# Kernel tuning notes

Hardware: AMD Instinct MI355X
Metric: run time of the kernel (lower is better)

Reference implementation:

```python
import jax, jax.numpy as jnp
import numpy as np

B, N, D, S, ITERS = 64, 2048, 256, 8, 3
SCALE = D ** -0.5
EPS_LN = 1e-5

def _ln(x, g, b):
    m = jnp.mean(x, axis=-1, keepdims=True)
    v = jnp.var(x, axis=-1, keepdims=True)
    return (x - m) / jnp.sqrt(v + EPS_LN) * g + b

def setup_inputs() -> dict:
    key = jax.random.key(0)
    ks = jax.random.split(key, 20)
    s = D ** -0.5
    f32 = jnp.float32
    return dict(
        x=jax.random.normal(ks[0], (B, N, D), f32),
        noise=jax.random.normal(ks[1], (B, S, D), f32),
        slots_mu=jax.random.normal(ks[2], (1, 1, D), f32),
        slots_sigma=jax.random.normal(ks[3], (1, 1, D), f32),
        Wq=jax.random.normal(ks[4], (D, D), f32) * s, bq=jnp.zeros((D,), f32),
        Wk=jax.random.normal(ks[5], (D, D), f32) * s, bk=jnp.zeros((D,), f32),
        Wv=jax.random.normal(ks[6], (D, D), f32) * s, bv=jnp.zeros((D,), f32),
        W_ih=jax.random.normal(ks[7], (3 * D, D), f32) * s, b_ih=jnp.zeros((3 * D,), f32),
        W_hh=jax.random.normal(ks[8], (3 * D, D), f32) * s, b_hh=jnp.zeros((3 * D,), f32),
        W1=jax.random.normal(ks[9], (D, D), f32) * s, b1=jnp.zeros((D,), f32),
        W2=jax.random.normal(ks[10], (D, D), f32) * s, b2=jnp.zeros((D,), f32),
        g_in=jnp.ones((D,), f32), be_in=jnp.zeros((D,), f32),
        g_sl=jnp.ones((D,), f32), be_sl=jnp.zeros((D,), f32),
        g_ff=jnp.ones((D,), f32), be_ff=jnp.zeros((D,), f32),
    )

def reference(x, noise, slots_mu, slots_sigma, Wq, bq, Wk, bk, Wv, bv,
              W_ih, b_ih, W_hh, b_hh, W1, b1, W2, b2,
              g_in, be_in, g_sl, be_sl, g_ff, be_ff):
    # slot init: mu + softplus(sigma) * noise  -> [B,S,D]
    slots = slots_mu + jax.nn.softplus(slots_sigma) * noise
    xn = _ln(x, g_in, be_in)
    k = xn @ Wk.T + bk  # [B,N,D]
    v = xn @ Wv.T + bv
    for _ in range(ITERS):
        prev = slots
        q = _ln(slots, g_sl, be_sl) @ Wq.T + bq  # [B,S,D]
        logits = jnp.einsum('bsd,bnd->bsn', q, k) * SCALE
        attn = jax.nn.softmax(logits, axis=-1) + 1e-8  # softmax over inputs, as in source
        attn = attn / jnp.sum(attn, axis=-1, keepdims=True)
        updates = jnp.einsum('bsn,bnd->bsd', attn, v)
        # GRUCell(input=updates, hidden=prev); torch gate order r,z,n
        gi = updates @ W_ih.T + b_ih
        gh = prev @ W_hh.T + b_hh
        ir, iz, i_n = jnp.split(gi, 3, axis=-1)
        hr, hz, h_n = jnp.split(gh, 3, axis=-1)
        r = jax.nn.sigmoid(ir + hr)
        z = jax.nn.sigmoid(iz + hz)
        n = jnp.tanh(i_n + r * h_n)
        slots = (1.0 - z) * n + z * prev
        # residual MLP
        h = jax.nn.relu(_ln(slots, g_ff, be_ff) @ W1.T + b1)
        slots = slots + (h @ W2.T + b2)
    return slots
```

## Files before the change

### kernel.cpp

```cpp
#include <hip/hip_runtime.h>
#include <cstddef>


#define BB 64
#define NN 2048
#define DD 256
#define NCH 8
#define CHK 256
#define NITER 3
#define XPITCH 264

typedef unsigned short u16;
typedef unsigned int u32;
typedef _Float16 h2 __attribute__((ext_vector_type(2)));
typedef _Float16 h4 __attribute__((ext_vector_type(4)));

#if defined(__has_builtin)
#if __has_builtin(__builtin_amdgcn_fdot2)
#define HAS_FDOT2 1
#endif
#endif

#ifdef HAS_FDOT2
#define FDOT2(a,b,c) __builtin_amdgcn_fdot2((a),(b),(c),false)
#else
#define FDOT2(a,b,c) fmaf((float)(a).y,(float)(b).y, fmaf((float)(a).x,(float)(b).x,(c)))
#endif

__device__ __forceinline__ h2 u2h2(u32 v){ union{u32 u; h2 h;} c; c.u=v; return c.h; }

__global__ __launch_bounds__(256) void kA(const float* __restrict__ x, const float* __restrict__ g_in,
                                          const float* __restrict__ be_in, u16* __restrict__ xn,
                                          const float* __restrict__ noise, const float* __restrict__ mu,
                                          const float* __restrict__ sig, float* __restrict__ S,
                                          const float* __restrict__ Wq, const float* __restrict__ Wk,
                                          const float* __restrict__ bq, const float* __restrict__ Wih,
                                          const float* __restrict__ Wv, const float* __restrict__ bv,
                                          const float* __restrict__ bih,
                                          float* __restrict__ Wqk, float* __restrict__ bqk,
                                          float* __restrict__ Wihv, float* __restrict__ bihv){
  __shared__ float col[256];
  const int t = threadIdx.x;
  const int blk = blockIdx.x;
  if(blk < 256){
    col[t] = Wq[t*256 + blk];
    __syncthreads();
    float acc = 0.f;
    #pragma unroll 4
    for(int j=0;j<256;j++) acc += col[j]*Wk[j*256+t];
    Wqk[blk*256+t] = acc * 0.0625f;
  } else if(blk < 1024){
    int c = blk - 256;
    col[t] = Wih[c*256+t];
    __syncthreads();
    float acc = 0.f;
    #pragma unroll 4
    for(int j=0;j<256;j++) acc += col[j]*Wv[j*256+t];
    Wihv[(size_t)c*256+t] = acc;
  } else if(blk < 1536){
    int i = (blk-1024)*256 + t;
    float sg = sig[t];
    float sp = fmaxf(sg, 0.f) + log1pf(expf(-fabsf(sg)));
    S[i] = mu[t] + sp * noise[i];
  } else if(blk == 1536){
    float acc = 0.f;
    for(int j=0;j<256;j++) acc += bq[j]*Wk[j*256+t];
    bqk[t] = acc * 0.0625f;
  } else if(blk == 1537){
    for(int c=t;c<768;c+=256){
      float acc = 0.f;
      for(int j=0;j<256;j++) acc += Wih[c*256+j]*bv[j];
      bihv[c] = acc + bih[c];
    }
  } else {
    int wave = t>>6, lane = t&63;
    size_t row = (size_t)(blk-1538)*4 + wave;
    float4 v = *(const float4*)(x + row*256 + lane*4);
    float s1 = v.x+v.y+v.z+v.w;
    float s2 = v.x*v.x + v.y*v.y + v.z*v.z + v.w*v.w;
    #pragma unroll
    for(int off=1; off<64; off<<=1){ s1 += __shfl_xor(s1,off); s2 += __shfl_xor(s2,off); }
    float m = s1*(1.f/256.f);
    float var = s2*(1.f/256.f) - m*m;
    float rs = rsqrtf(var + 1e-5f);
    float4 gg = *(const float4*)(g_in + lane*4);
    float4 bb = *(const float4*)(be_in + lane*4);
    union { h4 h; ushort4 s4; } pk;
    pk.h[0] = (_Float16)((v.x-m)*rs*gg.x + bb.x);
    pk.h[1] = (_Float16)((v.y-m)*rs*gg.y + bb.y);
    pk.h[2] = (_Float16)((v.z-m)*rs*gg.z + bb.z);
    pk.h[3] = (_Float16)((v.w-m)*rs*gg.w + bb.w);
    *(ushort4*)(xn + row*256 + lane*4) = pk.s4;
  }
}

__global__ __launch_bounds__(256) void kB(const float* __restrict__ Wihv, const float* __restrict__ Whh,
                                          const float* __restrict__ W1, const float* __restrict__ W2,
                                          float* __restrict__ WihvT, float* __restrict__ WhhT,
                                          float* __restrict__ W1T, float* __restrict__ W2T,
                                          const float* __restrict__ S0, const float* __restrict__ g_sl,
                                          const float* __restrict__ be_sl, const float* __restrict__ Wqk,
                                          const float* __restrict__ bqk, float* __restrict__ Qq){
  __shared__ float tile[64][65];
  __shared__ float lnA[8][256];
  const int blk = blockIdx.x, t = threadIdx.x;
  if(blk < 128){
    const float* src; float* dst; int R, C, tb;
    if(blk < 48){ src=Wihv; dst=WihvT; R=768; C=256; tb=blk; }
    else if(blk < 96){ src=Whh; dst=WhhT; R=768; C=256; tb=blk-48; }
    else if(blk < 112){ src=W1; dst=W1T; R=256; C=256; tb=blk-96; }
    else { src=W2; dst=W2T; R=256; C=256; tb=blk-112; }
    const int tilesC = C/64;
    const int r0 = (tb/tilesC)*64, c0 = (tb%tilesC)*64;
    const int x = t&63, y = t>>6;
    #pragma unroll
    for(int k=0;k<16;k++) tile[y*16+k][x] = src[(size_t)(r0+y*16+k)*C + c0+x];
    __syncthreads();
    #pragma unroll
    for(int k=0;k<16;k++) dst[(size_t)(c0+y*16+k)*R + r0+x] = tile[x][y*16+k];
    return;
  }
  const int w = t>>6, l = t&63;
  const int r0 = (blk-128)*8;
  #pragma unroll
  for(int rr=0; rr<2; rr++){
    int r = w*2 + rr;
    float4 v = *(const float4*)(S0 + (size_t)(r0+r)*256 + l*4);
    float s1 = v.x+v.y+v.z+v.w;
    float s2 = v.x*v.x+v.y*v.y+v.z*v.z+v.w*v.w;
    #pragma unroll
    for(int off=1; off<64; off<<=1){ s1 += __shfl_xor(s1,off); s2 += __shfl_xor(s2,off); }
    float m = s1*(1.f/256.f);
    float var = s2*(1.f/256.f) - m*m;
    float rs = rsqrtf(var + 1e-5f);
    float4 gg = *(const float4*)(g_sl + l*4);
    float4 bb = *(const float4*)(be_sl + l*4);
    float4 o;
    o.x=(v.x-m)*rs*gg.x+bb.x; o.y=(v.y-m)*rs*gg.y+bb.y;
    o.z=(v.z-m)*rs*gg.z+bb.z; o.w=(v.w-m)*rs*gg.w+bb.w;
    *(float4*)(&lnA[r][l*4]) = o;
  }
  __syncthreads();
  const int c4 = l*4;
  float acc[2][4] = {};
  #pragma unroll 2
  for(int k=0;k<256;k++){
    float4 wv = *(const float4*)(Wqk + (size_t)k*256 + c4);
    float a0 = lnA[2*w][k], a1 = lnA[2*w+1][k];
    acc[0][0]+=a0*wv.x; acc[0][1]+=a0*wv.y; acc[0][2]+=a0*wv.z; acc[0][3]+=a0*wv.w;
    acc[1][0]+=a1*wv.x; acc[1][1]+=a1*wv.y; acc[1][2]+=a1*wv.z; acc[1][3]+=a1*wv.w;
  }
  float4 bq4 = *(const float4*)(bqk + c4);
  #pragma unroll
  for(int rr=0; rr<2; rr++){
    float4 o;
    o.x=acc[rr][0]+bq4.x; o.y=acc[rr][1]+bq4.y; o.z=acc[rr][2]+bq4.z; o.w=acc[rr][3]+bq4.w;
    *(float4*)(Qq + (size_t)(r0+2*w+rr)*256 + c4) = o;
  }
}

__global__ __launch_bounds__(512) void k_attn(const float* __restrict__ Qq, const u16* __restrict__ xn,
                                              float* __restrict__ mP, float* __restrict__ lP,
                                              float* __restrict__ aP){
  __shared__ __align__(16) u16 xs[256*XPITCH];
  __shared__ h2 qs[8][128];
  __shared__ float plT[8][256];
  __shared__ float mS[8], lS[8];
  const int b = blockIdx.x, c = blockIdx.y, t = threadIdx.x;
  const int w = t>>6, l = t&63;
  {
    const uint4* xg4 = (const uint4*)(xn + ((size_t)b*NN + (size_t)c*CHK)*DD);
    #pragma unroll
    for(int k=0;k<16;k++){
      int idx = t + 512*k;
      int n = idx>>5, j = idx&31;
      *(uint4*)(xs + (size_t)n*XPITCH + j*8) = xg4[idx];
    }
  }
  for(int i=t; i<1024; i+=512){
    int s = i>>7, p = i&127;
    float a = Qq[b*2048 + s*256 + 2*p];
    float bq = Qq[b*2048 + s*256 + 2*p + 1];
    h2 hv; hv.x = (_Float16)a; hv.y = (_Float16)bq;
    qs[s][p] = hv;
  }
  __syncthreads();
  const int n = t & 255, sg = t >> 8;
  float lg[4]={0,0,0,0};
  {
    const u16* xr = xs + (size_t)n*XPITCH;
    #pragma unroll 4
    for(int d8=0; d8<32; ++d8){
      uint4 u = *(const uint4*)(xr + d8*8);
      h2 xa=u2h2(u.x), xb=u2h2(u.y), xc=u2h2(u.z), xd=u2h2(u.w);
      #pragma unroll
      for(int k=0;k<4;k++){
        const h2* qp = &qs[sg*4+k][d8*4];
        float acc = lg[k];
        acc = FDOT2(xa, qp[0], acc);
        acc = FDOT2(xb, qp[1], acc);
        acc = FDOT2(xc, qp[2], acc);
        acc = FDOT2(xd, qp[3], acc);
        lg[k] = acc;
      }
    }
    #pragma unroll
    for(int k=0;k<4;k++) plT[sg*4+k][n] = lg[k];
  }
  __syncthreads();
  {
    float mx = -1e30f;
    #pragma unroll
    for(int k=0;k<4;k++) mx = fmaxf(mx, plT[w][l + 64*k]);
    #pragma unroll
    for(int off=1; off<64; off<<=1) mx = fmaxf(mx, __shfl_xor(mx, off));
    if(l==0) mS[w] = mx;
  }
  __syncthreads();
  #pragma unroll
  for(int k=0;k<4;k++) plT[sg*4+k][n] = __expf(lg[k] - mS[sg*4+k]);
  __syncthreads();
  {
    float sm = 0.f;
    #pragma unroll
    for(int k=0;k<4;k++) sm += plT[w][l + 64*k];
    #pragma unroll
    for(int off=1; off<64; off<<=1) sm += __shfl_xor(sm, off);
    if(l==0) lS[w] = sm;
  }
  __syncthreads();
  const size_t pb = (size_t)(b*NCH + c)*8;
  {
    float4 a4 = {0.f,0.f,0.f,0.f};
    const u16* xq = xs + 4*l;
    #pragma unroll 8
    for(int nn=0; nn<256; ++nn){
      uint2 u = *(const uint2*)(xq + (size_t)nn*XPITCH);
      h2 ha=u2h2(u.x), hb=u2h2(u.y);
      float p = plT[w][nn];
      a4.x += p*(float)ha.x; a4.y += p*(float)ha.y;
      a4.z += p*(float)hb.x; a4.w += p*(float)hb.y;
    }
    *(float4*)(aP + (pb + w)*256 + l*4) = a4;
  }
  if(t<8){ mP[pb+t] = mS[t]; lP[pb+t] = lS[t]; }
}

union PostU {
  float Gt[2][4][768];
  struct { float Row[4][256]; float Ht[4][256]; float Lq[4][256]; } m;
};

__global__ __launch_bounds__(512) void k_post(const float* __restrict__ mP, const float* __restrict__ lP,
                                              const float* __restrict__ aP, const float* __restrict__ WihvT,
                                              const float* __restrict__ bihv, const float* __restrict__ WhhT,
                                              const float* __restrict__ bhh, const float* __restrict__ Sc,
                                              const float* __restrict__ g_ff, const float* __restrict__ be_ff,
                                              const float* __restrict__ W1T, const float* __restrict__ b1,
                                              const float* __restrict__ W2T, const float* __restrict__ b2,
                                              const float* __restrict__ g_sl, const float* __restrict__ be_sl,
                                              const float* __restrict__ Wqk, const float* __restrict__ bqk,
                                              float* __restrict__ Sout, float* __restrict__ Qq, int writeQ){
  __shared__ float Ut[4][256];
  __shared__ float Sp[4][256];
  __shared__ float Hp[2][4][256];
  __shared__ PostU uu;
  __shared__ float red2[4][2];
  const int t = threadIdx.x;
  const int r0 = blockIdx.x*4;
  const int b = r0>>3;
  const int w = t>>6, l = t&63;
  const int c = t&255, hh = t>>8;

  #pragma unroll
  for(int k=0;k<2;k++){
    int idx = t + 512*k;
    int r = idx>>8, cc = idx&255;
    int rr = r0 + r, ss = rr&7;
    const float* mpb = mP + b*64 + ss;
    const float* lpb = lP + b*64 + ss;
    float M = -1e30f;
    #pragma unroll
    for(int c8=0;c8<8;c8++) M = fmaxf(M, mpb[c8*8]);
    float wc[8]; float L = 0.f;
    #pragma unroll
    for(int c8=0;c8<8;c8++){ wc[c8] = __expf(mpb[c8*8] - M); L += lpb[c8*8]*wc[c8]; }
    float inv = 1.f/L;
    size_t base = ((size_t)b*64 + ss)*256 + cc;
    float u = 0.f;
    #pragma unroll
    for(int c8=0;c8<8;c8++) u += wc[c8]*aP[base + (size_t)c8*2048];
    Ut[r][cc] = u*inv;
    Sp[r][cc] = Sc[(size_t)rr*256 + cc];
  }
  __syncthreads();

  if(t < 384){
    const int mat = t/192, q4 = (t - mat*192)*4;
    const float* WT = mat ? WhhT : WihvT;
    const float* bb2 = mat ? bhh : bihv;
    const float (*A)[256] = mat ? Sp : Ut;
    float4 bias4 = *(const float4*)(bb2 + q4);
    float4 ac0 = bias4, ac1 = bias4, ac2 = bias4, ac3 = bias4;
    const float* wp = WT + q4;
    #pragma unroll 4
    for(int d=0; d<256; ++d){
      float4 wv = *(const float4*)(wp + (size_t)d*768);
      float a0=A[0][d], a1=A[1][d], a2=A[2][d], a3=A[3][d];
      ac0.x += a0*wv.x; ac0.y += a0*wv.y; ac0.z += a0*wv.z; ac0.w += a0*wv.w;
      ac1.x += a1*wv.x; ac1.y += a1*wv.y; ac1.z += a1*wv.z; ac1.w += a1*wv.w;
      ac2.x += a2*wv.x; ac2.y += a2*wv.y; ac2.z += a2*wv.z; ac2.w += a2*wv.w;
      ac3.x += a3*wv.x; ac3.y += a3*wv.y; ac3.z += a3*wv.z; ac3.w += a3*wv.w;
    }
    *(float4*)(&uu.Gt[mat][0][q4]) = ac0;
    *(float4*)(&uu.Gt[mat][1][q4]) = ac1;
    *(float4*)(&uu.Gt[mat][2][q4]) = ac2;
    *(float4*)(&uu.Gt[mat][3][q4]) = ac3;
  }
  __syncthreads();

  #pragma unroll
  for(int k=0;k<2;k++){
    int idx = t + 512*k;
    int r = idx>>8, cc = idx&255;
    float gir = uu.Gt[0][r][cc], giz = uu.Gt[0][r][256+cc], gin = uu.Gt[0][r][512+cc];
    float ghr = uu.Gt[1][r][cc], ghz = uu.Gt[1][r][256+cc], ghn = uu.Gt[1][r][512+cc];
    float rr2 = 1.f/(1.f + __expf(-(gir+ghr)));
    float zz = 1.f/(1.f + __expf(-(giz+ghz)));
    float nn = tanhf(gin + rr2*ghn);
    Ut[r][cc] = (1.f-zz)*nn + zz*Sp[r][cc];
  }
  __syncthreads();

  if(w < 4){
    float s1=0.f, s2=0.f;
    #pragma unroll
    for(int k2=0;k2<4;k2++){ float v = Ut[w][l + 64*k2]; s1 += v; s2 += v*v; }
    #pragma unroll
    for(int off=1; off<64; off<<=1){ s1 += __shfl_xor(s1,off); s2 += __shfl_xor(s2,off); }
    if(l==0){
      float m = s1*(1.f/256.f);
      float var = s2*(1.f/256.f) - m*m;
      red2[w][0] = m; red2[w][1] = rsqrtf(var + 1e-5f);
    }
  }
  __syncthreads();
  #pragma unroll
  for(int k=0;k<2;k++){
    int idx = t + 512*k;
    int r = idx>>8, cc = idx&255;
    uu.m.Row[r][cc] = (Ut[r][cc]-red2[r][0])*red2[r][1]*g_ff[cc] + be_ff[cc];
  }
  __syncthreads();

  {
    const float* w1 = W1T + (size_t)hh*128*256 + c;
    float a0 = hh ? 0.f : b1[c], a1=a0, a2=a0, a3=a0;
    const int dB = hh*128;
    #pragma unroll 8
    for(int d=0; d<128; ++d){
      float wv = w1[(size_t)d*256];
      a0 += uu.m.Row[0][dB+d]*wv;
      a1 += uu.m.Row[1][dB+d]*wv;
      a2 += uu.m.Row[2][dB+d]*wv;
      a3 += uu.m.Row[3][dB+d]*wv;
    }
    Hp[hh][0][c]=a0; Hp[hh][1][c]=a1; Hp[hh][2][c]=a2; Hp[hh][3][c]=a3;
  }
  __syncthreads();
  #pragma unroll
  for(int k=0;k<2;k++){
    int idx = t + 512*k;
    int r = idx>>8, cc = idx&255;
    uu.m.Ht[r][cc] = fmaxf(Hp[0][r][cc]+Hp[1][r][cc], 0.f);
  }
  __syncthreads();

  {
    const float* w2 = W2T + (size_t)hh*128*256 + c;
    float a0 = hh ? 0.f : b2[c], a1=a0, a2=a0, a3=a0;
    const int dB = hh*128;
    #pragma unroll 8
    for(int d=0; d<128; ++d){
      float wv = w2[(size_t)d*256];
      a0 += uu.m.Ht[0][dB+d]*wv;
      a1 += uu.m.Ht[1][dB+d]*wv;
      a2 += uu.m.Ht[2][dB+d]*wv;
      a3 += uu.m.Ht[3][dB+d]*wv;
    }
    Hp[hh][0][c]=a0; Hp[hh][1][c]=a1; Hp[hh][2][c]=a2; Hp[hh][3][c]=a3;
  }
  __syncthreads();
  if(t < 256){
    #pragma unroll
    for(int r=0;r<4;r++){
      float sn = Hp[0][r][c] + Hp[1][r][c] + Ut[r][c];
      Sout[(size_t)(r0+r)*256 + c] = sn;
      Ut[r][c] = sn;
    }
  }

  if(writeQ){
    __syncthreads();
    if(w < 4){
      float s1=0.f, s2=0.f;
      #pragma unroll
      for(int k2=0;k2<4;k2++){ float v = Ut[w][l + 64*k2]; s1 += v; s2 += v*v; }
      #pragma unroll
      for(int off=1; off<64; off<<=1){ s1 += __shfl_xor(s1,off); s2 += __shfl_xor(s2,off); }
      if(l==0){
        float m = s1*(1.f/256.f);
        float var = s2*(1.f/256.f) - m*m;
        red2[w][0] = m; red2[w][1] = rsqrtf(var + 1e-5f);
      }
    }
    __syncthreads();
    #pragma unroll
    for(int k=0;k<2;k++){
      int idx = t + 512*k;
      int r = idx>>8, cc = idx&255;
      uu.m.Lq[r][cc] = (Ut[r][cc]-red2[r][0])*red2[r][1]*g_sl[cc] + be_sl[cc];
    }
    __syncthreads();
    {
      const float* wq = Wqk + (size_t)hh*128*256 + c;
      float a0 = hh ? 0.f : bqk[c], a1=a0, a2=a0, a3=a0;
      const int dB = hh*128;
      #pragma unroll 8
      for(int d=0; d<128; ++d){
        float wv = wq[(size_t)d*256];
        a0 += uu.m.Lq[0][dB+d]*wv;
        a1 += uu.m.Lq[1][dB+d]*wv;
        a2 += uu.m.Lq[2][dB+d]*wv;
        a3 += uu.m.Lq[3][dB+d]*wv;
      }
      Hp[hh][0][c]=a0; Hp[hh][1][c]=a1; Hp[hh][2][c]=a2; Hp[hh][3][c]=a3;
    }
    __syncthreads();
    if(t < 256){
      #pragma unroll
      for(int r=0;r<4;r++)
        Qq[(size_t)(r0+r)*256 + c] = Hp[0][r][c] + Hp[1][r][c];
    }
  }
}

extern "C" void kernel_launch(void* const* d_in, const int* in_sizes, int n_in,
                              void* d_out, int out_size, void* d_ws, size_t ws_size,
                              hipStream_t stream){
  const float* x    = (const float*)d_in[0];
  const float* noise= (const float*)d_in[1];
  const float* mu   = (const float*)d_in[2];
  const float* sig  = (const float*)d_in[3];
  const float* Wq   = (const float*)d_in[4];
  const float* bq   = (const float*)d_in[5];
  const float* Wk   = (const float*)d_in[6];
  const float* Wv   = (const float*)d_in[8];
  const float* bv   = (const float*)d_in[9];
  const float* W_ih = (const float*)d_in[10];
  const float* b_ih = (const float*)d_in[11];
  const float* W_hh = (const float*)d_in[12];
  const float* b_hh = (const float*)d_in[13];
  const float* W1m  = (const float*)d_in[14];
  const float* b1v  = (const float*)d_in[15];
  const float* W2m  = (const float*)d_in[16];
  const float* b2v  = (const float*)d_in[17];
  const float* g_in = (const float*)d_in[18];
  const float* be_in= (const float*)d_in[19];
  const float* g_sl = (const float*)d_in[20];
  const float* be_sl= (const float*)d_in[21];
  const float* g_ff = (const float*)d_in[22];
  const float* be_ff= (const float*)d_in[23];

  char* p = (char*)d_ws;
  auto alloc = [&](size_t bytes)->char*{ char* q = p; p += (bytes + 255) & ~(size_t)255; return q; };
  u16*   xn    = (u16*)  alloc((size_t)BB*NN*DD*2);
  float* Wqk   = (float*)alloc(256*256*4);
  float* bqk   = (float*)alloc(256*4);
  float* Wihv  = (float*)alloc((size_t)768*256*4);
  float* WihvT = (float*)alloc((size_t)256*768*4);
  float* bihv  = (float*)alloc(768*4);
  float* WhhT  = (float*)alloc((size_t)256*768*4);
  float* W1T   = (float*)alloc(256*256*4);
  float* W2T   = (float*)alloc(256*256*4);
  float* S0    = (float*)alloc(512*256*4);
  float* S1    = (float*)alloc(512*256*4);
  float* Qq    = (float*)alloc(512*256*4);
  float* mP    = (float*)alloc(64*NCH*8*4);
  float* lP    = (float*)alloc(64*NCH*8*4);
  float* aP    = (float*)alloc((size_t)64*NCH*8*256*4);
  if((size_t)(p - (char*)d_ws) > ws_size) return;

  kA<<<34306, 256, 0, stream>>>(x, g_in, be_in, xn, noise, mu, sig, S0,
                                Wq, Wk, bq, W_ih, Wv, bv, b_ih, Wqk, bqk, Wihv, bihv);
  kB<<<192, 256, 0, stream>>>(Wihv, W_hh, W1m, W2m, WihvT, WhhT, W1T, W2T,
                              S0, g_sl, be_sl, Wqk, bqk, Qq);

  float* Sin = S0;
  float* Sping[2] = { S1, S0 };
  for(int it=0; it<NITER; ++it){
    float* Sout = (it==NITER-1) ? (float*)d_out : Sping[it&1];
    k_attn<<<dim3(64, NCH), 512, 0, stream>>>(Qq, xn, mP, lP, aP);
    k_post<<<128, 512, 0, stream>>>(mP, lP, aP, WihvT, bihv, WhhT, b_hh, Sin, g_ff, be_ff,
                                    W1T, b1v, W2T, b2v, g_sl, be_sl, Wqk, bqk,
                                    Sout, Qq, (it<NITER-1) ? 1 : 0);
    Sin = Sout;
  }
}
```

Baseline: 326.8 us.

## Fuse input LayerNorm into attention kernel, dropping the fp16 xn buffer

Removes the separate LayerNorm pass that wrote a half-precision normalized copy of x. Instead, each attention block normalizes its chunk of x directly into shared memory on every iteration. This avoids the xn write and the separate large launch. In exchange, each of the three attention passes now reads fp32 x (twice the bytes) and redoes the LayerNorm.

```diff
diff --git a/kernel.cpp b/kernel.cpp
--- a/kernel.cpp
+++ b/kernel.cpp
@@ -29,9 +29,7 @@
 
 __device__ __forceinline__ h2 u2h2(u32 v){ union{u32 u; h2 h;} c; c.u=v; return c.h; }
 
-__global__ __launch_bounds__(256) void kA(const float* __restrict__ x, const float* __restrict__ g_in,
-                                          const float* __restrict__ be_in, u16* __restrict__ xn,
-                                          const float* __restrict__ noise, const float* __restrict__ mu,
+__global__ __launch_bounds__(256) void kA(const float* __restrict__ noise, const float* __restrict__ mu,
                                           const float* __restrict__ sig, float* __restrict__ S,
                                           const float* __restrict__ Wq, const float* __restrict__ Wk,
                                           const float* __restrict__ bq, const float* __restrict__ Wih,
@@ -66,31 +64,12 @@
     float acc = 0.f;
     for(int j=0;j<256;j++) acc += bq[j]*Wk[j*256+t];
     bqk[t] = acc * 0.0625f;
-  } else if(blk == 1537){
+  } else {
     for(int c=t;c<768;c+=256){
       float acc = 0.f;
       for(int j=0;j<256;j++) acc += Wih[c*256+j]*bv[j];
       bihv[c] = acc + bih[c];
     }
-  } else {
-    int wave = t>>6, lane = t&63;
-    size_t row = (size_t)(blk-1538)*4 + wave;
-    float4 v = *(const float4*)(x + row*256 + lane*4);
-    float s1 = v.x+v.y+v.z+v.w;
-    float s2 = v.x*v.x + v.y*v.y + v.z*v.z + v.w*v.w;
-    #pragma unroll
-    for(int off=1; off<64; off<<=1){ s1 += __shfl_xor(s1,off); s2 += __shfl_xor(s2,off); }
-    float m = s1*(1.f/256.f);
-    float var = s2*(1.f/256.f) - m*m;
-    float rs = rsqrtf(var + 1e-5f);
-    float4 gg = *(const float4*)(g_in + lane*4);
-    float4 bb = *(const float4*)(be_in + lane*4);
-    union { h4 h; ushort4 s4; } pk;
-    pk.h[0] = (_Float16)((v.x-m)*rs*gg.x + bb.x);
-    pk.h[1] = (_Float16)((v.y-m)*rs*gg.y + bb.y);
-    pk.h[2] = (_Float16)((v.z-m)*rs*gg.z + bb.z);
-    pk.h[3] = (_Float16)((v.w-m)*rs*gg.w + bb.w);
-    *(ushort4*)(xn + row*256 + lane*4) = pk.s4;
   }
 }
 
@@ -159,7 +138,8 @@
   }
 }
 
-__global__ __launch_bounds__(512) void k_attn(const float* __restrict__ Qq, const u16* __restrict__ xn,
+__global__ __launch_bounds__(512) void k_attn(const float* __restrict__ x, const float* __restrict__ g_in,
+                                              const float* __restrict__ be_in, const float* __restrict__ Qq,
                                               float* __restrict__ mP, float* __restrict__ lP,
                                               float* __restrict__ aP){
   __shared__ __align__(16) u16 xs[256*XPITCH];
@@ -169,12 +149,26 @@
   const int b = blockIdx.x, c = blockIdx.y, t = threadIdx.x;
   const int w = t>>6, l = t&63;
   {
-    const uint4* xg4 = (const uint4*)(xn + ((size_t)b*NN + (size_t)c*CHK)*DD);
-    #pragma unroll
-    for(int k=0;k<16;k++){
-      int idx = t + 512*k;
-      int n = idx>>5, j = idx&31;
-      *(uint4*)(xs + (size_t)n*XPITCH + j*8) = xg4[idx];
+    const float* xb = x + ((size_t)b*NN + (size_t)c*CHK)*DD;
+    float4 gg = *(const float4*)(g_in + l*4);
+    float4 bb = *(const float4*)(be_in + l*4);
+    #pragma unroll 4
+    for(int k=0;k<32;k++){
+      int row = w + 8*k;
+      float4 v = *(const float4*)(xb + (size_t)row*256 + l*4);
+      float s1 = v.x+v.y+v.z+v.w;
+      float s2 = v.x*v.x + v.y*v.y + v.z*v.z + v.w*v.w;
+      #pragma unroll
+      for(int off=1; off<64; off<<=1){ s1 += __shfl_xor(s1,off); s2 += __shfl_xor(s2,off); }
+      float m = s1*(1.f/256.f);
+      float var = s2*(1.f/256.f) - m*m;
+      float rs = rsqrtf(var + 1e-5f);
+      union { h4 h; uint2 u2v; } pk;
+      pk.h[0] = (_Float16)((v.x-m)*rs*gg.x + bb.x);
+      pk.h[1] = (_Float16)((v.y-m)*rs*gg.y + bb.y);
+      pk.h[2] = (_Float16)((v.z-m)*rs*gg.z + bb.z);
+      pk.h[3] = (_Float16)((v.w-m)*rs*gg.w + bb.w);
+      *(uint2*)(xs + (size_t)row*XPITCH + l*4) = pk.u2v;
     }
   }
   for(int i=t; i<1024; i+=512){
@@ -474,7 +468,6 @@
 
   char* p = (char*)d_ws;
   auto alloc = [&](size_t bytes)->char*{ char* q = p; p += (bytes + 255) & ~(size_t)255; return q; };
-  u16*   xn    = (u16*)  alloc((size_t)BB*NN*DD*2);
   float* Wqk   = (float*)alloc(256*256*4);
   float* bqk   = (float*)alloc(256*4);
   float* Wihv  = (float*)alloc((size_t)768*256*4);
@@ -491,8 +484,8 @@
   float* aP    = (float*)alloc((size_t)64*NCH*8*256*4);
   if((size_t)(p - (char*)d_ws) > ws_size) return;
 
-  kA<<<34306, 256, 0, stream>>>(x, g_in, be_in, xn, noise, mu, sig, S0,
-                                Wq, Wk, bq, W_ih, Wv, bv, b_ih, Wqk, bqk, Wihv, bihv);
+  kA<<<1538, 256, 0, stream>>>(noise, mu, sig, S0, Wq, Wk, bq, W_ih, Wv, bv, b_ih,
+                               Wqk, bqk, Wihv, bihv);
   kB<<<192, 256, 0, stream>>>(Wihv, W_hh, W1m, W2m, WihvT, WhhT, W1T, W2T,
                               S0, g_sl, be_sl, Wqk, bqk, Qq);
 
@@ -500,7 +493,7 @@
   float* Sping[2] = { S1, S0 };
   for(int it=0; it<NITER; ++it){
     float* Sout = (it==NITER-1) ? (float*)d_out : Sping[it&1];
-    k_attn<<<dim3(64, NCH), 512, 0, stream>>>(Qq, xn, mP, lP, aP);
+    k_attn<<<dim3(64, NCH), 512, 0, stream>>>(x, g_in, be_in, Qq, mP, lP, aP);
     k_post<<<128, 512, 0, stream>>>(mP, lP, aP, WihvT, bihv, WhhT, b_hh, Sin, g_ff, be_ff,
                                     W1T, b1v, W2T, b2v, g_sl, be_sl, Wqk, bqk,
                                     Sout, Qq, (it<NITER-1) ? 1 : 0);
```

Result: slower. 355.1 us (+8.7%).
